# Kernel optimization log

Hardware: AMD Instinct MI355X
Metric: run time of the kernel (lower is better)

## Reference

```python
import jax, jax.numpy as jnp
import numpy as np


def _init(key, shape, fan_in):
    return jax.random.normal(key, shape, jnp.float32) * (1.0 / np.sqrt(fan_in))


def setup_inputs() -> dict:
    key = jax.random.key(0)
    ks = jax.random.split(key, 12)
    b, n, vd, ad, sd, hd = 32, 2048, 512, 128, 128, 64
    return {
        'vfeat': jax.random.normal(ks[0], (b, n, vd), jnp.float32),
        'afeat': jax.random.normal(ks[1], (b, n, ad), jnp.float32),
        'vfc_w': _init(ks[2], (ad, vd), vd), 'vfc_b': jnp.zeros((ad,), jnp.float32),
        'afc_w': _init(ks[3], (ad, ad), ad), 'afc_b': jnp.zeros((ad,), jnp.float32),
        'am_v_w': _init(ks[4], (sd, sd), sd), 'am_v_b': jnp.zeros((sd,), jnp.float32),
        'am_a_w': _init(ks[5], (sd, sd), sd), 'am_a_b': jnp.zeros((sd,), jnp.float32),
        'am_o_w': _init(ks[6], (1, sd), sd), 'am_o_b': jnp.zeros((1,), jnp.float32),
        'V_w': _init(ks[7], (hd, sd), sd), 'V_b': jnp.zeros((hd,), jnp.float32),
        'W_w': _init(ks[8], (1, hd), hd), 'W_b': jnp.zeros((1,), jnp.float32),
        'cls_w': _init(ks[9], (2, sd), sd), 'cls_b': jnp.zeros((2,), jnp.float32),
    }


def reference(vfeat, afeat, vfc_w, vfc_b, afc_w, afc_b,
              am_v_w, am_v_b, am_a_w, am_a_b, am_o_w, am_o_b,
              V_w, V_b, W_w, W_b, cls_w, cls_b):
    relu = jax.nn.relu
    # vfc / afc projections (dropout is identity in eval mode)
    vo1 = relu(jnp.einsum('bnd,kd->bnk', vfeat, vfc_w) + vfc_b)  # (b,n,128)
    ax = relu(jnp.einsum('bnd,kd->bnk', afeat, afc_w) + afc_b)   # (b,n,128)
    # AM(128): additive gated cross-modal attention: out = sigmoid(Wo tanh(Wv v + Wa a)) * a
    h = jnp.tanh(jnp.einsum('bnk,jk->bnj', vo1, am_v_w) + am_v_b
                 + jnp.einsum('bnk,jk->bnj', ax, am_a_w) + am_a_b)
    att = jax.nn.sigmoid(jnp.einsum('bnj,oj->bno', h, am_o_w) + am_o_b)  # (b,n,1)
    ffeat = att * ax + vo1  # attfeat + vo1, (b,n,128)
    # NOTE: original uses self.V for BOTH f_v and f_u (source bug kept)
    f_v = relu(jnp.einsum('bnk,hk->bnh', ffeat, V_w) + V_b)  # (b,n,64)
    f_u = f_v
    # W is affine with no nonlinearity on (fv_i + fu_j), so
    # W(fv_i + fu_j) = w.fv_i + w.fu_j + b  -- exact rank-1 decomposition
    s_v = f_v @ W_w[0]  # (b,n)
    s_u = f_u @ W_w[0]  # (b,n)
    pair = s_v[:, :, None] + s_u[:, None, :] + W_b[0]  # (b,n_i,n_j)
    p = jax.nn.softmax(pair, axis=1)  # F.softmax(scores, 0) per bag: over i
    scores = p.mean(axis=2)  # mean over j -> (b,n)
    # eval mode: training-only softmax over dim 2 skipped
    zfeat = jnp.einsum('bn,bnk->bk', scores, ffeat)  # (b,128)
    logits = zfeat @ cls_w.T + cls_b  # (b,2)
    return scores, logits
```

## Files before the change

### kernel.cpp

```cpp
#include <hip/hip_runtime.h>
#include <cstddef>
#include <cstdint>


typedef __attribute__((ext_vector_type(8))) short short8;
typedef __attribute__((ext_vector_type(4))) float float4v;

#define MFMA16(a, b, c) __builtin_amdgcn_mfma_f32_16x16x32_bf16((a), (b), (c), 0, 0, 0)

__device__ __forceinline__ unsigned short f2bf(float f) {
    union { float f; unsigned u; } v; v.f = f;
    unsigned r = (v.u + 0x7fffu + ((v.u >> 16) & 1u)) >> 16;
    return (unsigned short)r;
}
__device__ __forceinline__ float bf2f(unsigned short h) {
    union { unsigned u; float f; } v; v.u = ((unsigned)h) << 16;
    return v.f;
}
__device__ __forceinline__ float bf2f_s(short h) { return bf2f((unsigned short)h); }

__device__ __forceinline__ void bfsplit(float x, short& h, short& l) {
    union { float f; unsigned u; } v; v.f = x;
    h = (short)(v.u >> 16);
    union { unsigned u; float f; } hv; hv.u = v.u & 0xffff0000u;
    union { float f; unsigned u; } lv; lv.f = x - hv.f;
    l = (short)(lv.u >> 16);
}

__device__ __forceinline__ float tanh_fast(float x) {
    float e = __builtin_exp2f(x * 2.885390081777927f);
    return 1.f - 2.f / (e + 1.f);
}
__device__ __forceinline__ float sigmoid_fast(float x) {
    return 1.f / (1.f + __builtin_exp2f(-x * 1.4426950408889634f));
}

__device__ __forceinline__ void gload_lds16(const void* g, void* l) {
#if __has_builtin(__builtin_amdgcn_global_load_lds)
    __builtin_amdgcn_global_load_lds(
        (const __attribute__((address_space(1))) unsigned int*)g,
        (__attribute__((address_space(3))) unsigned int*)l, 16, 0, 0);
#else
    *(uint4*)l = *(const uint4*)g;
#endif
}

__global__ __launch_bounds__(256)
void prep(const float* __restrict__ vfc_w, const float* __restrict__ afc_w,
          const float* __restrict__ am_v_w, const float* __restrict__ am_a_w,
          const float* __restrict__ V_w,
          unsigned short* __restrict__ W1h, unsigned short* __restrict__ W1l,
          unsigned short* __restrict__ W1bh, unsigned short* __restrict__ W1bl,
          unsigned short* __restrict__ W2v, unsigned short* __restrict__ W2a,
          unsigned short* __restrict__ W3)
{
    int t = blockIdx.x * 256 + threadIdx.x;
    if (t < 65536) {
        int j = t & 7, lane = (t >> 3) & 63, ks = (t >> 9) & 15, nf = (t >> 13) & 7;
        int n = (lane & 15) + 16 * nf, k = ks * 32 + (lane >> 4) * 8 + j;
        float x = vfc_w[n * 512 + k];
        unsigned short h = f2bf(x);
        W1h[t] = h; W1l[t] = f2bf(x - bf2f(h));
    } else if (t < 81920) {
        int u = t - 65536;
        int j = u & 7, lane = (u >> 3) & 63, ks = (u >> 9) & 3, nf = (u >> 11) & 7;
        int n = (lane & 15) + 16 * nf, k = ks * 32 + (lane >> 4) * 8 + j;
        float x = afc_w[n * 128 + k];
        unsigned short h = f2bf(x);
        W1bh[u] = h; W1bl[u] = f2bf(x - bf2f(h));
    } else if (t < 98304) {
        int u = t - 81920;
        int j = u & 7, lane = (u >> 3) & 63, ks = (u >> 9) & 3, nf = (u >> 11) & 7;
        int n = (lane & 15) + 16 * nf, k = ks * 32 + (lane >> 4) * 8 + j;
        W2v[u] = f2bf(am_v_w[n * 128 + k]);
    } else if (t < 114688) {
        int u = t - 98304;
        int j = u & 7, lane = (u >> 3) & 63, ks = (u >> 9) & 3, nf = (u >> 11) & 7;
        int n = (lane & 15) + 16 * nf, k = ks * 32 + (lane >> 4) * 8 + j;
        W2a[u] = f2bf(am_a_w[n * 128 + k]);
    } else if (t < 122880) {
        int u = t - 114688;
        int j = u & 7, lane = (u >> 3) & 63, ks = (u >> 9) & 3, nf = (u >> 11) & 3;
        int n = (lane & 15) + 16 * nf, k = ks * 32 + (lane >> 4) * 8 + j;
        W3[u] = f2bf(V_w[n * 128 + k]);
    }
}

__global__ __launch_bounds__(256, 2)
void milA(const float* __restrict__ vfeat, const float* __restrict__ afeat,
          const float* __restrict__ vfc_b, const float* __restrict__ afc_b,
          const float* __restrict__ am_v_b, const float* __restrict__ am_a_b,
          const float* __restrict__ am_o_w, const float* __restrict__ am_o_b,
          const float* __restrict__ V_b, const float* __restrict__ W_w,
          const unsigned short* __restrict__ W1h, const unsigned short* __restrict__ W1l,
          const unsigned short* __restrict__ W1bh, const unsigned short* __restrict__ W1bl,
          const unsigned short* __restrict__ W2v, const unsigned short* __restrict__ W2a,
          const unsigned short* __restrict__ W3,
          float* __restrict__ ffeat_out, float* __restrict__ s_out)
{
    __shared__ __align__(16) unsigned short vo1s[16384];
    __shared__ __align__(16) unsigned short axs[16384];
    __shared__ __align__(16) unsigned short bstage[8192];

    const int tid = threadIdx.x;
    const int lane = tid & 63, wid = tid >> 6;
    const int lr = lane & 15, lg = lane >> 4;
    const int row0 = blockIdx.x * 128 + wid * 32;

    float b1[8], b1b[8], bias2[8], wo[8];
#pragma unroll
    for (int nf = 0; nf < 8; ++nf) {
        const int c = lr + 16 * nf;
        b1[nf] = vfc_b[c];
        b1b[nf] = afc_b[c];
        bias2[nf] = am_v_b[c] + am_a_b[c];
        wo[nf] = am_o_w[c];
    }
    const float ob = am_o_b[0];

    float4v acc1[2][8];
#pragma unroll
    for (int rf = 0; rf < 2; ++rf)
#pragma unroll
        for (int nf = 0; nf < 8; ++nf)
#pragma unroll
            for (int i = 0; i < 4; ++i) acc1[rf][nf][i] = 0.f;

    {
        const float* ap0 = vfeat + (size_t)(row0 + lr) * 512 + lg * 8;
        const float* ap1 = ap0 + (size_t)16 * 512;
        float4 acur[2][2];
        acur[0][0] = *(const float4*)(ap0);
        acur[0][1] = *(const float4*)(ap0 + 4);
        acur[1][0] = *(const float4*)(ap1);
        acur[1][1] = *(const float4*)(ap1 + 4);

        for (int ks = 0; ks < 16; ++ks) {
            __syncthreads();
#pragma unroll
            for (int i = 0; i < 4; ++i) {
                const int idx = wid * 4 + i;
                const unsigned short* src = (idx < 8)
                    ? W1h + (size_t)(idx * 16 + ks) * 512
                    : W1l + (size_t)((idx - 8) * 16 + ks) * 512;
                gload_lds16(src + (size_t)lane * 8, &bstage[idx * 512 + lane * 8]);
            }
            __syncthreads();

            float4 anxt[2][2];
            if (ks < 15) {
                anxt[0][0] = *(const float4*)(ap0 + (ks + 1) * 32);
                anxt[0][1] = *(const float4*)(ap0 + (ks + 1) * 32 + 4);
                anxt[1][0] = *(const float4*)(ap1 + (ks + 1) * 32);
                anxt[1][1] = *(const float4*)(ap1 + (ks + 1) * 32 + 4);
            }
            short8 ah[2], al[2];
#pragma unroll
            for (int rf = 0; rf < 2; ++rf) {
                const float xs[8] = {acur[rf][0].x, acur[rf][0].y, acur[rf][0].z, acur[rf][0].w,
                                     acur[rf][1].x, acur[rf][1].y, acur[rf][1].z, acur[rf][1].w};
#pragma unroll
                for (int j = 0; j < 8; ++j) {
                    short h, l; bfsplit(xs[j], h, l);
                    ah[rf][j] = h; al[rf][j] = l;
                }
            }
#pragma unroll
            for (int nf = 0; nf < 8; ++nf) {
                const short8 bh = *(const short8*)&bstage[nf * 512 + lane * 8];
                const short8 bl = *(const short8*)&bstage[4096 + nf * 512 + lane * 8];
#pragma unroll
                for (int rf = 0; rf < 2; ++rf) {
                    acc1[rf][nf] = MFMA16(ah[rf], bh, acc1[rf][nf]);
                    acc1[rf][nf] = MFMA16(ah[rf], bl, acc1[rf][nf]);
                    acc1[rf][nf] = MFMA16(al[rf], bh, acc1[rf][nf]);
                }
            }
            if (ks < 15) {
#pragma unroll
                for (int rf = 0; rf < 2; ++rf) {
                    acur[rf][0] = anxt[rf][0];
                    acur[rf][1] = anxt[rf][1];
                }
            }
        }
    }
#pragma unroll
    for (int rf = 0; rf < 2; ++rf)
#pragma unroll
        for (int nf = 0; nf < 8; ++nf)
#pragma unroll
            for (int r = 0; r < 4; ++r) {
                float v = fmaxf(acc1[rf][nf][r] + b1[nf], 0.f);
                acc1[rf][nf][r] = v;
                const int row = rf * 16 + lg * 4 + r;
                const int col = lr + 16 * nf;
                vo1s[wid * 4096 + row * 128 + (col ^ ((row & 7) << 3))] = f2bf(v);
            }

    float4v acc1b[2][8];
#pragma unroll
    for (int rf = 0; rf < 2; ++rf)
#pragma unroll
        for (int nf = 0; nf < 8; ++nf)
#pragma unroll
            for (int i = 0; i < 4; ++i) acc1b[rf][nf][i] = 0.f;

    {
        const float* ap0 = afeat + (size_t)(row0 + lr) * 128 + lg * 8;
        const float* ap1 = ap0 + (size_t)16 * 128;
        float4 acur[2][2];
        acur[0][0] = *(const float4*)(ap0);
        acur[0][1] = *(const float4*)(ap0 + 4);
        acur[1][0] = *(const float4*)(ap1);
        acur[1][1] = *(const float4*)(ap1 + 4);

        for (int ks = 0; ks < 4; ++ks) {
            __syncthreads();
#pragma unroll
            for (int i = 0; i < 4; ++i) {
                const int idx = wid * 4 + i;
                const unsigned short* src = (idx < 8)
                    ? W1bh + (size_t)(idx * 4 + ks) * 512
                    : W1bl + (size_t)((idx - 8) * 4 + ks) * 512;
                gload_lds16(src + (size_t)lane * 8, &bstage[idx * 512 + lane * 8]);
            }
            __syncthreads();

            float4 anxt[2][2];
            if (ks < 3) {
                anxt[0][0] = *(const float4*)(ap0 + (ks + 1) * 32);
                anxt[0][1] = *(const float4*)(ap0 + (ks + 1) * 32 + 4);
                anxt[1][0] = *(const float4*)(ap1 + (ks + 1) * 32);
                anxt[1][1] = *(const float4*)(ap1 + (ks + 1) * 32 + 4);
            }
            short8 ah[2], al[2];
#pragma unroll
            for (int rf = 0; rf < 2; ++rf) {
                const float xs[8] = {acur[rf][0].x, acur[rf][0].y, acur[rf][0].z, acur[rf][0].w,
                                     acur[rf][1].x, acur[rf][1].y, acur[rf][1].z, acur[rf][1].w};
#pragma unroll
                for (int j = 0; j < 8; ++j) {
                    short h, l; bfsplit(xs[j], h, l);
                    ah[rf][j] = h; al[rf][j] = l;
                }
            }
#pragma unroll
            for (int nf = 0; nf < 8; ++nf) {
                const short8 bh = *(const short8*)&bstage[nf * 512 + lane * 8];
                const short8 bl = *(const short8*)&bstage[4096 + nf * 512 + lane * 8];
#pragma unroll
                for (int rf = 0; rf < 2; ++rf) {
                    acc1b[rf][nf] = MFMA16(ah[rf], bh, acc1b[rf][nf]);
                    acc1b[rf][nf] = MFMA16(ah[rf], bl, acc1b[rf][nf]);
                    acc1b[rf][nf] = MFMA16(al[rf], bh, acc1b[rf][nf]);
                }
            }
            if (ks < 3) {
#pragma unroll
                for (int rf = 0; rf < 2; ++rf) {
                    acur[rf][0] = anxt[rf][0];
                    acur[rf][1] = anxt[rf][1];
                }
            }
        }
    }
#pragma unroll
    for (int rf = 0; rf < 2; ++rf)
#pragma unroll
        for (int nf = 0; nf < 8; ++nf)
#pragma unroll
            for (int r = 0; r < 4; ++r) {
                float v = fmaxf(acc1b[rf][nf][r] + b1b[nf], 0.f);
                acc1b[rf][nf][r] = v;
                const int row = rf * 16 + lg * 4 + r;
                const int col = lr + 16 * nf;
                axs[wid * 4096 + row * 128 + (col ^ ((row & 7) << 3))] = f2bf(v);
            }

    float4v acc2[2][8];
#pragma unroll
    for (int rf = 0; rf < 2; ++rf)
#pragma unroll
        for (int nf = 0; nf < 8; ++nf)
#pragma unroll
            for (int i = 0; i < 4; ++i) acc2[rf][nf][i] = 0.f;

    for (int ks = 0; ks < 4; ++ks) {
        __syncthreads();
#pragma unroll
        for (int i = 0; i < 2; ++i) {
            const int idx = wid * 2 + i;
            gload_lds16(W2v + (size_t)(idx * 4 + ks) * 512 + lane * 8,
                        &bstage[idx * 512 + lane * 8]);
        }
        __syncthreads();
        short8 a2[2];
#pragma unroll
        for (int rf = 0; rf < 2; ++rf) {
            const int row = rf * 16 + lr;
            a2[rf] = *(const short8*)&vo1s[wid * 4096 + row * 128 +
                                           ((ks * 32 + lg * 8) ^ ((row & 7) << 3))];
        }
#pragma unroll
        for (int nf = 0; nf < 8; ++nf) {
            const short8 b = *(const short8*)&bstage[nf * 512 + lane * 8];
#pragma unroll
            for (int rf = 0; rf < 2; ++rf) acc2[rf][nf] = MFMA16(a2[rf], b, acc2[rf][nf]);
        }
    }
    for (int ks = 0; ks < 4; ++ks) {
        __syncthreads();
#pragma unroll
        for (int i = 0; i < 2; ++i) {
            const int idx = wid * 2 + i;
            gload_lds16(W2a + (size_t)(idx * 4 + ks) * 512 + lane * 8,
                        &bstage[idx * 512 + lane * 8]);
        }
        __syncthreads();
        short8 a2[2];
#pragma unroll
        for (int rf = 0; rf < 2; ++rf) {
            const int row = rf * 16 + lr;
            a2[rf] = *(const short8*)&axs[wid * 4096 + row * 128 +
                                          ((ks * 32 + lg * 8) ^ ((row & 7) << 3))];
        }
#pragma unroll
        for (int nf = 0; nf < 8; ++nf) {
            const short8 b = *(const short8*)&bstage[nf * 512 + lane * 8];
#pragma unroll
            for (int rf = 0; rf < 2; ++rf) acc2[rf][nf] = MFMA16(a2[rf], b, acc2[rf][nf]);
        }
    }

    float attc[2][4];
#pragma unroll
    for (int rf = 0; rf < 2; ++rf)
#pragma unroll
        for (int r = 0; r < 4; ++r) {
            float p = 0.f;
#pragma unroll
            for (int nf = 0; nf < 8; ++nf)
                p += tanh_fast(acc2[rf][nf][r] + bias2[nf]) * wo[nf];
            p += __shfl_xor(p, 1);
            p += __shfl_xor(p, 2);
            p += __shfl_xor(p, 4);
            p += __shfl_xor(p, 8);
            attc[rf][r] = sigmoid_fast(p + ob);
        }

#pragma unroll
    for (int rf = 0; rf < 2; ++rf)
#pragma unroll
        for (int nf = 0; nf < 8; ++nf)
#pragma unroll
            for (int r = 0; r < 4; ++r)
                ffeat_out[(size_t)(row0 + rf * 16 + lg * 4 + r) * 128 + lr + 16 * nf] =
                    attc[rf][r] * acc1b[rf][nf][r] + acc1[rf][nf][r];

    float attv[2];
    {
        const int srcl = (lr >> 2) << 4;
#pragma unroll
        for (int rf = 0; rf < 2; ++rf) {
            const float b0 = __shfl(attc[rf][0], srcl);
            const float b1 = __shfl(attc[rf][1], srcl);
            const float b2 = __shfl(attc[rf][2], srcl);
            const float b3 = __shfl(attc[rf][3], srcl);
            attv[rf] = (lr & 2) ? ((lr & 1) ? b3 : b2) : ((lr & 1) ? b1 : b0);
        }
    }

    float4v acc3[2][4];
#pragma unroll
    for (int rf = 0; rf < 2; ++rf)
#pragma unroll
        for (int nf = 0; nf < 4; ++nf)
#pragma unroll
            for (int i = 0; i < 4; ++i) acc3[rf][nf][i] = 0.f;

    for (int ks = 0; ks < 4; ++ks) {
        __syncthreads();
        gload_lds16(W3 + (size_t)(wid * 4 + ks) * 512 + lane * 8,
                    &bstage[wid * 512 + lane * 8]);
        __syncthreads();
        short8 a3[2];
#pragma unroll
        for (int rf = 0; rf < 2; ++rf) {
            const int row = rf * 16 + lr;
            const int sidx = wid * 4096 + row * 128 + ((ks * 32 + lg * 8) ^ ((row & 7) << 3));
            const short8 x8 = *(const short8*)&axs[sidx];
            const short8 v8 = *(const short8*)&vo1s[sidx];
#pragma unroll
            for (int j = 0; j < 8; ++j) {
                float f = attv[rf] * bf2f_s(x8[j]) + bf2f_s(v8[j]);
                a3[rf][j] = (short)f2bf(f);
            }
        }
#pragma unroll
        for (int nf = 0; nf < 4; ++nf) {
            const short8 b = *(const short8*)&bstage[nf * 512 + lane * 8];
#pragma unroll
            for (int rf = 0; rf < 2; ++rf) acc3[rf][nf] = MFMA16(a3[rf], b, acc3[rf][nf]);
        }
    }

    float vb3[4], ww3[4];
#pragma unroll
    for (int nf = 0; nf < 4; ++nf) {
        const int c = lr + 16 * nf;
        vb3[nf] = V_b[c];
        ww3[nf] = W_w[c];
    }
#pragma unroll
    for (int rf = 0; rf < 2; ++rf)
#pragma unroll
        for (int r = 0; r < 4; ++r) {
            float q = 0.f;
#pragma unroll
            for (int nf = 0; nf < 4; ++nf)
                q += fmaxf(acc3[rf][nf][r] + vb3[nf], 0.f) * ww3[nf];
            q += __shfl_xor(q, 1);
            q += __shfl_xor(q, 2);
            q += __shfl_xor(q, 4);
            q += __shfl_xor(q, 8);
            if (lr == 0) s_out[row0 + rf * 16 + lg * 4 + r] = q;
        }
}

__device__ __forceinline__ float wred_sum(float v) {
#pragma unroll
    for (int m = 32; m >= 1; m >>= 1) v += __shfl_xor(v, m);
    return v;
}
__device__ __forceinline__ float wred_max(float v) {
#pragma unroll
    for (int m = 32; m >= 1; m >>= 1) v = fmaxf(v, __shfl_xor(v, m));
    return v;
}

__global__ __launch_bounds__(256)
void milB1(const float* __restrict__ s_in, float* __restrict__ scores_out)
{
    __shared__ float red[4];
    const int t = threadIdx.x, b = blockIdx.x, w = t >> 6;
    const float* sb = s_in + (size_t)b * 2048;

    float v[8];
#pragma unroll
    for (int q = 0; q < 8; ++q) v[q] = sb[q * 256 + t];
    float m = v[0];
#pragma unroll
    for (int q = 1; q < 8; ++q) m = fmaxf(m, v[q]);
    m = wred_max(m);
    if ((t & 63) == 0) red[w] = m;
    __syncthreads();
    const float bm = fmaxf(fmaxf(red[0], red[1]), fmaxf(red[2], red[3]));

    float e[8], sum = 0.f;
#pragma unroll
// ... 58 lines not shown
    const float* vfc_w  = (const float*)d_in[2];
    const float* vfc_b  = (const float*)d_in[3];
    const float* afc_w  = (const float*)d_in[4];
    const float* afc_b  = (const float*)d_in[5];
    const float* am_v_w = (const float*)d_in[6];
    const float* am_v_b = (const float*)d_in[7];
    const float* am_a_w = (const float*)d_in[8];
    const float* am_a_b = (const float*)d_in[9];
    const float* am_o_w = (const float*)d_in[10];
    const float* am_o_b = (const float*)d_in[11];
    const float* V_w    = (const float*)d_in[12];
    const float* V_b    = (const float*)d_in[13];
    const float* W_w    = (const float*)d_in[14];
    const float* cls_w  = (const float*)d_in[16];
    const float* cls_b  = (const float*)d_in[17];

    float* scores = (float*)d_out;
    float* logits = (float*)d_out + 32 * 2048;

    char* ws = (char*)d_ws;
    float* ffeat_ws = (float*)ws;
    float* s_ws     = (float*)(ws + 33554432);
    float* parts_ws = (float*)(ws + 33816576);
    unsigned short* W1h  = (unsigned short*)(ws + 33947648);
    unsigned short* W1l  = W1h + 65536;
    unsigned short* W1bh = W1l + 65536;
    unsigned short* W1bl = W1bh + 16384;
    unsigned short* W2v  = W1bl + 16384;
    unsigned short* W2a  = W2v + 16384;
    unsigned short* W3   = W2a + 16384;

    prep<<<480, 256, 0, stream>>>(vfc_w, afc_w, am_v_w, am_a_w, V_w,
                                  W1h, W1l, W1bh, W1bl, W2v, W2a, W3);
    milA<<<512, 256, 0, stream>>>(vfeat, afeat, vfc_b, afc_b, am_v_b, am_a_b,
                                  am_o_w, am_o_b, V_b, W_w,
                                  W1h, W1l, W1bh, W1bl, W2v, W2a, W3,
                                  ffeat_ws, s_ws);
    milB1<<<32, 256, 0, stream>>>(s_ws, scores);
    milB2<<<256, 256, 0, stream>>>(scores, ffeat_ws, parts_ws);
    milB3<<<32, 128, 0, stream>>>(parts_ws, cls_w, cls_b, logits);
}
```

Before: 91.96 us.

## Halve rows per wave in milA to raise occupancy and merge W2 staging loops

Each wave in milA now handles 16 rows instead of 32, so the grid doubles to 1024 blocks and LDS and register usage per block roughly halve. Launch bounds move to 3 blocks per CU. The A-operand prefetch becomes two steps deep, the W2v and W2a passes share one staged loop, and all of W3 is loaded once before the final GEMM instead of per k-step. The aim is more occupancy and fewer barriers to hide global-load latency, at the cost of reloading each weight tile for half as many rows, which doubles weight staging traffic.

```diff
diff --git a/kernel.cpp b/kernel.cpp
--- a/kernel.cpp
+++ b/kernel.cpp
@@ -86,7 +86,7 @@
     }
 }
 
-__global__ __launch_bounds__(256, 2)
+__global__ __launch_bounds__(256, 3)
 void milA(const float* __restrict__ vfeat, const float* __restrict__ afeat,
           const float* __restrict__ vfc_b, const float* __restrict__ afc_b,
           const float* __restrict__ am_v_b, const float* __restrict__ am_a_b,
@@ -98,42 +98,26 @@
           const unsigned short* __restrict__ W3,
           float* __restrict__ ffeat_out, float* __restrict__ s_out)
 {
-    __shared__ __align__(16) unsigned short vo1s[16384];
-    __shared__ __align__(16) unsigned short axs[16384];
+    __shared__ __align__(16) unsigned short vo1s[8192];
+    __shared__ __align__(16) unsigned short axs[8192];
     __shared__ __align__(16) unsigned short bstage[8192];
 
     const int tid = threadIdx.x;
     const int lane = tid & 63, wid = tid >> 6;
     const int lr = lane & 15, lg = lane >> 4;
-    const int row0 = blockIdx.x * 128 + wid * 32;
-
-    float b1[8], b1b[8], bias2[8], wo[8];
-#pragma unroll
-    for (int nf = 0; nf < 8; ++nf) {
-        const int c = lr + 16 * nf;
-        b1[nf] = vfc_b[c];
-        b1b[nf] = afc_b[c];
-        bias2[nf] = am_v_b[c] + am_a_b[c];
-        wo[nf] = am_o_w[c];
-    }
-    const float ob = am_o_b[0];
-
-    float4v acc1[2][8];
-#pragma unroll
-    for (int rf = 0; rf < 2; ++rf)
-#pragma unroll
-        for (int nf = 0; nf < 8; ++nf)
-#pragma unroll
-            for (int i = 0; i < 4; ++i) acc1[rf][nf][i] = 0.f;
+    const int row0 = blockIdx.x * 64 + wid * 16;
+
+    float4v acc1[8];
+#pragma unroll
+    for (int nf = 0; nf < 8; ++nf)
+#pragma unroll
+        for (int i = 0; i < 4; ++i) acc1[nf][i] = 0.f;
 
     {
-        const float* ap0 = vfeat + (size_t)(row0 + lr) * 512 + lg * 8;
-        const float* ap1 = ap0 + (size_t)16 * 512;
-        float4 acur[2][2];
-        acur[0][0] = *(const float4*)(ap0);
-        acur[0][1] = *(const float4*)(ap0 + 4);
-        acur[1][0] = *(const float4*)(ap1);
-        acur[1][1] = *(const float4*)(ap1 + 4);
+        const float* ap = vfeat + (size_t)(row0 + lr) * 512 + lg * 8;
+        float4 a0[2], a1[2], a2[2];
+        a0[0] = *(const float4*)(ap);      a0[1] = *(const float4*)(ap + 4);
+        a1[0] = *(const float4*)(ap + 32); a1[1] = *(const float4*)(ap + 36);
 
         for (int ks = 0; ks < 16; ++ks) {
             __syncthreads();
@@ -147,73 +131,56 @@
             }
             __syncthreads();
 
-            float4 anxt[2][2];
-            if (ks < 15) {
-                anxt[0][0] = *(const float4*)(ap0 + (ks + 1) * 32);
-                anxt[0][1] = *(const float4*)(ap0 + (ks + 1) * 32 + 4);
-                anxt[1][0] = *(const float4*)(ap1 + (ks + 1) * 32);
-                anxt[1][1] = *(const float4*)(ap1 + (ks + 1) * 32 + 4);
-            }
-            short8 ah[2], al[2];
-#pragma unroll
-            for (int rf = 0; rf < 2; ++rf) {
-                const float xs[8] = {acur[rf][0].x, acur[rf][0].y, acur[rf][0].z, acur[rf][0].w,
-                                     acur[rf][1].x, acur[rf][1].y, acur[rf][1].z, acur[rf][1].w};
+            if (ks < 14) {
+                a2[0] = *(const float4*)(ap + (ks + 2) * 32);
+                a2[1] = *(const float4*)(ap + (ks + 2) * 32 + 4);
+            }
+            short8 ah, al;
+            {
+                const float xs[8] = {a0[0].x, a0[0].y, a0[0].z, a0[0].w,
+                                     a0[1].x, a0[1].y, a0[1].z, a0[1].w};
 #pragma unroll
                 for (int j = 0; j < 8; ++j) {
                     short h, l; bfsplit(xs[j], h, l);
-                    ah[rf][j] = h; al[rf][j] = l;
+                    ah[j] = h; al[j] = l;
                 }
             }
 #pragma unroll
             for (int nf = 0; nf < 8; ++nf) {
                 const short8 bh = *(const short8*)&bstage[nf * 512 + lane * 8];
                 const short8 bl = *(const short8*)&bstage[4096 + nf * 512 + lane * 8];
-#pragma unroll
-                for (int rf = 0; rf < 2; ++rf) {
-                    acc1[rf][nf] = MFMA16(ah[rf], bh, acc1[rf][nf]);
-                    acc1[rf][nf] = MFMA16(ah[rf], bl, acc1[rf][nf]);
-                    acc1[rf][nf] = MFMA16(al[rf], bh, acc1[rf][nf]);
-                }
-            }
-            if (ks < 15) {
-#pragma unroll
-                for (int rf = 0; rf < 2; ++rf) {
-                    acur[rf][0] = anxt[rf][0];
-                    acur[rf][1] = anxt[rf][1];
-                }
-            }
-        }
-    }
-#pragma unroll
-    for (int rf = 0; rf < 2; ++rf)
-#pragma unroll
-        for (int nf = 0; nf < 8; ++nf)
-#pragma unroll
-            for (int r = 0; r < 4; ++r) {
-                float v = fmaxf(acc1[rf][nf][r] + b1[nf], 0.f);
-                acc1[rf][nf][r] = v;
-                const int row = rf * 16 + lg * 4 + r;
-                const int col = lr + 16 * nf;
-                vo1s[wid * 4096 + row * 128 + (col ^ ((row & 7) << 3))] = f2bf(v);
-            }
-
-    float4v acc1b[2][8];
-#pragma unroll
-    for (int rf = 0; rf < 2; ++rf)
-#pragma unroll
-        for (int nf = 0; nf < 8; ++nf)
-#pragma unroll
-            for (int i = 0; i < 4; ++i) acc1b[rf][nf][i] = 0.f;
+                acc1[nf] = MFMA16(ah, bh, acc1[nf]);
+                acc1[nf] = MFMA16(ah, bl, acc1[nf]);
+                acc1[nf] = MFMA16(al, bh, acc1[nf]);
+            }
+            a0[0] = a1[0]; a0[1] = a1[1];
+            a1[0] = a2[0]; a1[1] = a2[1];
+        }
+    }
+#pragma unroll
+    for (int nf = 0; nf < 8; ++nf) {
+        const float bb = vfc_b[lr + 16 * nf];
+#pragma unroll
+        for (int r = 0; r < 4; ++r) {
+            float v = fmaxf(acc1[nf][r] + bb, 0.f);
+            acc1[nf][r] = v;
+            const int row = lg * 4 + r;
+            const int col = lr + 16 * nf;
+            vo1s[wid * 2048 + row * 128 + (col ^ ((row & 7) << 3))] = f2bf(v);
+        }
+    }
+
+    float4v acc1b[8];
+#pragma unroll
+    for (int nf = 0; nf < 8; ++nf)
+#pragma unroll
+        for (int i = 0; i < 4; ++i) acc1b[nf][i] = 0.f;
 
     {
-        const float* ap0 = afeat + (size_t)(row0 + lr) * 128 + lg * 8;
-        const float* ap1 = ap0 + (size_t)16 * 128;
-        float4 acur[2][2];
-        acur[0][0] = *(const float4*)(ap0);
-        acur[0][1] = *(const float4*)(ap0 + 4);
-        acur[1][0] = *(const float4*)(ap1);
-        acur[1][1] = *(const float4*)(ap1 + 4);
+        const float* ap = afeat + (size_t)(row0 + lr) * 128 + lg * 8;
+        float4 a0[2], a1[2], a2[2];
+        a0[0] = *(const float4*)(ap);      a0[1] = *(const float4*)(ap + 4);
+        a1[0] = *(const float4*)(ap + 32); a1[1] = *(const float4*)(ap + 36);
 
         for (int ks = 0; ks < 4; ++ks) {
             __syncthreads();
@@ -227,205 +194,169 @@
             }
             __syncthreads();
 
-            float4 anxt[2][2];
-            if (ks < 3) {
-                anxt[0][0] = *(const float4*)(ap0 + (ks + 1) * 32);
-                anxt[0][1] = *(const float4*)(ap0 + (ks + 1) * 32 + 4);
-                anxt[1][0] = *(const float4*)(ap1 + (ks + 1) * 32);
-                anxt[1][1] = *(const float4*)(ap1 + (ks + 1) * 32 + 4);
-            }
-            short8 ah[2], al[2];
-#pragma unroll
-            for (int rf = 0; rf < 2; ++rf) {
-                const float xs[8] = {acur[rf][0].x, acur[rf][0].y, acur[rf][0].z, acur[rf][0].w,
-                                     acur[rf][1].x, acur[rf][1].y, acur[rf][1].z, acur[rf][1].w};
+            if (ks < 2) {
+                a2[0] = *(const float4*)(ap + (ks + 2) * 32);
+                a2[1] = *(const float4*)(ap + (ks + 2) * 32 + 4);
+            }
+            short8 ah, al;
+            {
+                const float xs[8] = {a0[0].x, a0[0].y, a0[0].z, a0[0].w,
+                                     a0[1].x, a0[1].y, a0[1].z, a0[1].w};
 #pragma unroll
                 for (int j = 0; j < 8; ++j) {
                     short h, l; bfsplit(xs[j], h, l);
-                    ah[rf][j] = h; al[rf][j] = l;
+                    ah[j] = h; al[j] = l;
                 }
             }
 #pragma unroll
             for (int nf = 0; nf < 8; ++nf) {
                 const short8 bh = *(const short8*)&bstage[nf * 512 + lane * 8];
                 const short8 bl = *(const short8*)&bstage[4096 + nf * 512 + lane * 8];
-#pragma unroll
-                for (int rf = 0; rf < 2; ++rf) {
-                    acc1b[rf][nf] = MFMA16(ah[rf], bh, acc1b[rf][nf]);
-                    acc1b[rf][nf] = MFMA16(ah[rf], bl, acc1b[rf][nf]);
-                    acc1b[rf][nf] = MFMA16(al[rf], bh, acc1b[rf][nf]);
-                }
-            }
-            if (ks < 3) {
-#pragma unroll
-                for (int rf = 0; rf < 2; ++rf) {
-                    acur[rf][0] = anxt[rf][0];
-                    acur[rf][1] = anxt[rf][1];
-                }
-            }
-        }
-    }
-#pragma unroll
-    for (int rf = 0; rf < 2; ++rf)
-#pragma unroll
-        for (int nf = 0; nf < 8; ++nf)
-#pragma unroll
-            for (int r = 0; r < 4; ++r) {
-                float v = fmaxf(acc1b[rf][nf][r] + b1b[nf], 0.f);
-                acc1b[rf][nf][r] = v;
-                const int row = rf * 16 + lg * 4 + r;
-                const int col = lr + 16 * nf;
-                axs[wid * 4096 + row * 128 + (col ^ ((row & 7) << 3))] = f2bf(v);
-            }
-
-    float4v acc2[2][8];
-#pragma unroll
-    for (int rf = 0; rf < 2; ++rf)
-#pragma unroll
-        for (int nf = 0; nf < 8; ++nf)
-#pragma unroll
-            for (int i = 0; i < 4; ++i) acc2[rf][nf][i] = 0.f;
+                acc1b[nf] = MFMA16(ah, bh, acc1b[nf]);
+                acc1b[nf] = MFMA16(ah, bl, acc1b[nf]);
+                acc1b[nf] = MFMA16(al, bh, acc1b[nf]);
+            }
+            a0[0] = a1[0]; a0[1] = a1[1];
+            a1[0] = a2[0]; a1[1] = a2[1];
+        }
+    }
+#pragma unroll
+    for (int nf = 0; nf < 8; ++nf) {
+        const float bb = afc_b[lr + 16 * nf];
+#pragma unroll
+        for (int r = 0; r < 4; ++r) {
+            float v = fmaxf(acc1b[nf][r] + bb, 0.f);
+            acc1b[nf][r] = v;
+            const int row = lg * 4 + r;
+            const int col = lr + 16 * nf;
+            axs[wid * 2048 + row * 128 + (col ^ ((row & 7) << 3))] = f2bf(v);
+        }
+    }
+
+    float4v acc2[8];
+#pragma unroll
+    for (int nf = 0; nf < 8; ++nf)
+#pragma unroll
+        for (int i = 0; i < 4; ++i) acc2[nf][i] = 0.f;
 
     for (int ks = 0; ks < 4; ++ks) {
         __syncthreads();
 #pragma unroll
-        for (int i = 0; i < 2; ++i) {
-            const int idx = wid * 2 + i;
-            gload_lds16(W2v + (size_t)(idx * 4 + ks) * 512 + lane * 8,
-                        &bstage[idx * 512 + lane * 8]);
+        for (int i = 0; i < 4; ++i) {
+            const int idx = wid * 4 + i;
+            const unsigned short* src = (idx < 8)
+                ? W2v + (size_t)(idx * 4 + ks) * 512
+                : W2a + (size_t)((idx - 8) * 4 + ks) * 512;
+            gload_lds16(src + (size_t)lane * 8, &bstage[idx * 512 + lane * 8]);
         }
         __syncthreads();
-        short8 a2[2];
-#pragma unroll
-        for (int rf = 0; rf < 2; ++rf) {
-            const int row = rf * 16 + lr;
-            a2[rf] = *(const short8*)&vo1s[wid * 4096 + row * 128 +
-                                           ((ks * 32 + lg * 8) ^ ((row & 7) << 3))];
-        }
+        const int rdoff = (ks * 32 + lg * 8) ^ ((lr & 7) << 3);
+        const short8 a2v = *(const short8*)&vo1s[wid * 2048 + lr * 128 + rdoff];
+        const short8 a2a = *(const short8*)&axs[wid * 2048 + lr * 128 + rdoff];
 #pragma unroll
         for (int nf = 0; nf < 8; ++nf) {
-            const short8 b = *(const short8*)&bstage[nf * 512 + lane * 8];
-#pragma unroll
-            for (int rf = 0; rf < 2; ++rf) acc2[rf][nf] = MFMA16(a2[rf], b, acc2[rf][nf]);
-        }
-    }
-    for (int ks = 0; ks < 4; ++ks) {
-        __syncthreads();
-#pragma unroll
-        for (int i = 0; i < 2; ++i) {
-            const int idx = wid * 2 + i;
-            gload_lds16(W2a + (size_t)(idx * 4 + ks) * 512 + lane * 8,
-                        &bstage[idx * 512 + lane * 8]);
-        }
-        __syncthreads();
-        short8 a2[2];
-#pragma unroll
-        for (int rf = 0; rf < 2; ++rf) {
-            const int row = rf * 16 + lr;
-            a2[rf] = *(const short8*)&axs[wid * 4096 + row * 128 +
-                                          ((ks * 32 + lg * 8) ^ ((row & 7) << 3))];
-        }
+            const short8 bv = *(const short8*)&bstage[nf * 512 + lane * 8];
+            const short8 ba = *(const short8*)&bstage[4096 + nf * 512 + lane * 8];
+            acc2[nf] = MFMA16(a2v, bv, acc2[nf]);
+            acc2[nf] = MFMA16(a2a, ba, acc2[nf]);
+        }
+    }
+
+    __syncthreads();
+#pragma unroll
+    for (int i = 0; i < 4; ++i) {
+        const int idx = wid * 4 + i;
+        gload_lds16(W3 + (size_t)idx * 512 + lane * 8, &bstage[idx * 512 + lane * 8]);
+    }
+
+    float attc[4];
+    {
+        float bias2[8], wo[8];
 #pragma unroll
         for (int nf = 0; nf < 8; ++nf) {
-            const short8 b = *(const short8*)&bstage[nf * 512 + lane * 8];
-#pragma unroll
-            for (int rf = 0; rf < 2; ++rf) acc2[rf][nf] = MFMA16(a2[rf], b, acc2[rf][nf]);
-        }
-    }
-
-    float attc[2][4];
-#pragma unroll
-    for (int rf = 0; rf < 2; ++rf)
+            const int c = lr + 16 * nf;
+            bias2[nf] = am_v_b[c] + am_a_b[c];
+            wo[nf] = am_o_w[c];
+        }
+        const float ob = am_o_b[0];
 #pragma unroll
         for (int r = 0; r < 4; ++r) {
             float p = 0.f;
 #pragma unroll
             for (int nf = 0; nf < 8; ++nf)
-                p += tanh_fast(acc2[rf][nf][r] + bias2[nf]) * wo[nf];
+                p += tanh_fast(acc2[nf][r] + bias2[nf]) * wo[nf];
             p += __shfl_xor(p, 1);
             p += __shfl_xor(p, 2);
             p += __shfl_xor(p, 4);
             p += __shfl_xor(p, 8);
-            attc[rf][r] = sigmoid_fast(p + ob);
-        }
-
-#pragma unroll
-    for (int rf = 0; rf < 2; ++rf)
-#pragma unroll
-        for (int nf = 0; nf < 8; ++nf)
-#pragma unroll
-            for (int r = 0; r < 4; ++r)
-                ffeat_out[(size_t)(row0 + rf * 16 + lg * 4 + r) * 128 + lr + 16 * nf] =
-                    attc[rf][r] * acc1b[rf][nf][r] + acc1[rf][nf][r];
-
-    float attv[2];
+            attc[r] = sigmoid_fast(p + ob);
+        }
+    }
+
+#pragma unroll
+    for (int nf = 0; nf < 8; ++nf)
+#pragma unroll
+        for (int r = 0; r < 4; ++r)
+            ffeat_out[(size_t)(row0 + lg * 4 + r) * 128 + lr + 16 * nf] =
+                attc[r] * acc1b[nf][r] + acc1[nf][r];
+
+    float attv;
     {
         const int srcl = (lr >> 2) << 4;
-#pragma unroll
-        for (int rf = 0; rf < 2; ++rf) {
-            const float b0 = __shfl(attc[rf][0], srcl);
-            const float b1 = __shfl(attc[rf][1], srcl);
-            const float b2 = __shfl(attc[rf][2], srcl);
-            const float b3 = __shfl(attc[rf][3], srcl);
-            attv[rf] = (lr & 2) ? ((lr & 1) ? b3 : b2) : ((lr & 1) ? b1 : b0);
-        }
-    }
-
-    float4v acc3[2][4];
-#pragma unroll
-    for (int rf = 0; rf < 2; ++rf)
-#pragma unroll
-        for (int nf = 0; nf < 4; ++nf)
-#pragma unroll
-            for (int i = 0; i < 4; ++i) acc3[rf][nf][i] = 0.f;
-
+        const float b0 = __shfl(attc[0], srcl);
+        const float b1 = __shfl(attc[1], srcl);
+        const float b2 = __shfl(attc[2], srcl);
+        const float b3 = __shfl(attc[3], srcl);
+        attv = (lr & 2) ? ((lr & 1) ? b3 : b2) : ((lr & 1) ? b1 : b0);
+    }
+
+    __syncthreads();
+
+    float4v acc3[4];
+#pragma unroll
+    for (int nf = 0; nf < 4; ++nf)
+#pragma unroll
+        for (int i = 0; i < 4; ++i) acc3[nf][i] = 0.f;
+
+#pragma unroll
     for (int ks = 0; ks < 4; ++ks) {
-        __syncthreads();
-        gload_lds16(W3 + (size_t)(wid * 4 + ks) * 512 + lane * 8,
-                    &bstage[wid * 512 + lane * 8]);
-        __syncthreads();
-        short8 a3[2];
-#pragma unroll
-        for (int rf = 0; rf < 2; ++rf) {
-            const int row = rf * 16 + lr;
-            const int sidx = wid * 4096 + row * 128 + ((ks * 32 + lg * 8) ^ ((row & 7) << 3));
-            const short8 x8 = *(const short8*)&axs[sidx];
-            const short8 v8 = *(const short8*)&vo1s[sidx];
-#pragma unroll
-            for (int j = 0; j < 8; ++j) {
-                float f = attv[rf] * bf2f_s(x8[j]) + bf2f_s(v8[j]);
-                a3[rf][j] = (short)f2bf(f);
-            }
+        const int rdoff = (ks * 32 + lg * 8) ^ ((lr & 7) << 3);
+        const short8 x8 = *(const short8*)&axs[wid * 2048 + lr * 128 + rdoff];
+        const short8 v8 = *(const short8*)&vo1s[wid * 2048 + lr * 128 + rdoff];
+        short8 a3;
+#pragma unroll
+        for (int j = 0; j < 8; ++j) {
+            float f = attv * bf2f_s(x8[j]) + bf2f_s(v8[j]);
+            a3[j] = (short)f2bf(f);
         }
 #pragma unroll
         for (int nf = 0; nf < 4; ++nf) {
-            const short8 b = *(const short8*)&bstage[nf * 512 + lane * 8];
-#pragma unroll
-            for (int rf = 0; rf < 2; ++rf) acc3[rf][nf] = MFMA16(a3[rf], b, acc3[rf][nf]);
-        }
-    }
-
-    float vb3[4], ww3[4];
-#pragma unroll
-    for (int nf = 0; nf < 4; ++nf) {
-        const int c = lr + 16 * nf;
-        vb3[nf] = V_b[c];
-        ww3[nf] = W_w[c];
-    }
-#pragma unroll
-    for (int rf = 0; rf < 2; ++rf)
+            const short8 b = *(const short8*)&bstage[(nf * 4 + ks) * 512 + lane * 8];
+            acc3[nf] = MFMA16(a3, b, acc3[nf]);
+        }
+    }
+
+    {
+        float vb3[4], ww3[4];
+#pragma unroll
+        for (int nf = 0; nf < 4; ++nf) {
+            const int c = lr + 16 * nf;
+            vb3[nf] = V_b[c];
+            ww3[nf] = W_w[c];
+        }
 #pragma unroll
         for (int r = 0; r < 4; ++r) {
             float q = 0.f;
 #pragma unroll
             for (int nf = 0; nf < 4; ++nf)
-                q += fmaxf(acc3[rf][nf][r] + vb3[nf], 0.f) * ww3[nf];
+                q += fmaxf(acc3[nf][r] + vb3[nf], 0.f) * ww3[nf];
             q += __shfl_xor(q, 1);
             q += __shfl_xor(q, 2);
             q += __shfl_xor(q, 4);
             q += __shfl_xor(q, 8);
-            if (lr == 0) s_out[row0 + rf * 16 + lg * 4 + r] = q;
-        }
+            if (lr == 0) s_out[row0 + lg * 4 + r] = q;
+        }
+    }
 }
 
 __device__ __forceinline__ float wred_sum(float v) {
@@ -550,10 +481,10 @@
 
     prep<<<480, 256, 0, stream>>>(vfc_w, afc_w, am_v_w, am_a_w, V_w,
                                   W1h, W1l, W1bh, W1bl, W2v, W2a, W3);
-    milA<<<512, 256, 0, stream>>>(vfeat, afeat, vfc_b, afc_b, am_v_b, am_a_b,
-                                  am_o_w, am_o_b, V_b, W_w,
-                                  W1h, W1l, W1bh, W1bl, W2v, W2a, W3,
-                                  ffeat_ws, s_ws);
+    milA<<<1024, 256, 0, stream>>>(vfeat, afeat, vfc_b, afc_b, am_v_b, am_a_b,
+                                   am_o_w, am_o_b, V_b, W_w,
+                                   W1h, W1l, W1bh, W1bl, W2v, W2a, W3,
+                                   ffeat_ws, s_ws);
     milB1<<<32, 256, 0, stream>>>(s_ws, scores);
     milB2<<<256, 256, 0, stream>>>(scores, ffeat_ws, parts_ws);
     milB3<<<32, 128, 0, stream>>>(parts_ws, cls_w, cls_b, logits);
```

New measurement: 88.82 us. -3.4%, faster.

## Pipeline weight staging with triple-buffered LDS and unified slice schedule in milA

Applied to the files above, without the earlier changes.

Replaces the per-k-step double-syncthreads weight staging with a triple-buffered LDS ring, a unified 25-slice schedule spanning all GEMM phases, and inline-asm activation loads kept two steps ahead, synchronized with explicit vmcnt waits and single barriers. It fuses the two AM GEMM loops into one interleaved loop and prestages W3 so the final GEMM needs no barriers. Launch bounds drop to one block per SM to afford the larger LDS and register footprint. The aim is to hide global load latency and cut barrier count, at the cost of lower occupancy and fragile hand-counted vmcnt values.

```diff
diff --git a/kernel.cpp b/kernel.cpp
--- a/kernel.cpp
+++ b/kernel.cpp
@@ -7,6 +7,9 @@
 typedef __attribute__((ext_vector_type(4))) float float4v;
 
 #define MFMA16(a, b, c) __builtin_amdgcn_mfma_f32_16x16x32_bf16((a), (b), (c), 0, 0, 0)
+#define VMCNT(n) asm volatile("s_waitcnt vmcnt(" #n ")" ::: "memory")
+#define BARRIER() __builtin_amdgcn_s_barrier()
+#define SCHED0() __builtin_amdgcn_sched_barrier(0)
 
 __device__ __forceinline__ unsigned short f2bf(float f) {
     union { float f; unsigned u; } v; v.f = f;
@@ -43,6 +46,11 @@
 #else
     *(uint4*)l = *(const uint4*)g;
 #endif
+}
+
+__device__ __forceinline__ void gload4(float4v& d, const float* p) {
+    asm volatile("global_load_dwordx4 %0, %1, off"
+                 : "=&v"(d) : "v"(p) : "memory");
 }
 
 __global__ __launch_bounds__(256)
@@ -86,7 +94,7 @@
     }
 }
 
-__global__ __launch_bounds__(256, 2)
+__global__ __launch_bounds__(256, 1)
 void milA(const float* __restrict__ vfeat, const float* __restrict__ afeat,
           const float* __restrict__ vfc_b, const float* __restrict__ afc_b,
           const float* __restrict__ am_v_b, const float* __restrict__ am_a_b,
@@ -98,25 +106,70 @@
           const unsigned short* __restrict__ W3,
           float* __restrict__ ffeat_out, float* __restrict__ s_out)
 {
+    __shared__ __align__(16) unsigned short bstage[3][8192];
     __shared__ __align__(16) unsigned short vo1s[16384];
     __shared__ __align__(16) unsigned short axs[16384];
-    __shared__ __align__(16) unsigned short bstage[8192];
 
     const int tid = threadIdx.x;
     const int lane = tid & 63, wid = tid >> 6;
     const int lr = lane & 15, lg = lane >> 4;
     const int row0 = blockIdx.x * 128 + wid * 32;
 
-    float b1[8], b1b[8], bias2[8], wo[8];
-#pragma unroll
-    for (int nf = 0; nf < 8; ++nf) {
-        const int c = lr + 16 * nf;
-        b1[nf] = vfc_b[c];
-        b1b[nf] = afc_b[c];
-        bias2[nf] = am_v_b[c] + am_a_b[c];
-        wo[nf] = am_o_w[c];
-    }
-    const float ob = am_o_b[0];
+    const float* apv0 = vfeat + (size_t)(row0 + lr) * 512 + lg * 8;
+    const float* apv1 = apv0 + (size_t)16 * 512;
+    const float* apa0 = afeat + (size_t)(row0 + lr) * 128 + lg * 8;
+    const float* apa1 = apa0 + (size_t)16 * 128;
+
+    auto stage16 = [&](const unsigned short* th, const unsigned short* tl,
+                       int nks, int ks, int buf) {
+#pragma unroll
+        for (int i = 0; i < 4; ++i) {
+            const int f = wid * 4 + i;
+            const int nf = f & 7;
+            const unsigned short* src = ((f >> 3) ? tl : th)
+                + ((size_t)(nf * nks + ks)) * 512 + (size_t)lane * 8;
+            gload_lds16(src, &bstage[buf][f * 512 + lane * 8]);
+        }
+    };
+    auto stage_slice = [&](int s, int buf) {
+        if (s < 16)      stage16(W1h,  W1l,  16, s,      buf);
+        else if (s < 20) stage16(W1bh, W1bl, 4,  s - 16, buf);
+        else if (s < 24) stage16(W2v,  W2a,  4,  s - 20, buf);
+        else if (s == 24) {
+#pragma unroll
+            for (int i = 0; i < 4; ++i) {
+                const int f = wid * 4 + i;
+                gload_lds16(W3 + (size_t)f * 512 + lane * 8,
+                            &bstage[buf][f * 512 + lane * 8]);
+            }
+        }
+    };
+
+    float4v a0[4], a1[4], a2[4];
+    auto issueA = [&](float4v (&a)[4], int b) {
+        const float *p0, *p1;
+        if (b < 16)      { p0 = apv0 + b * 32;        p1 = apv1 + b * 32; }
+        else if (b < 20) { p0 = apa0 + (b - 16) * 32; p1 = apa1 + (b - 16) * 32; }
+        else return;
+        gload4(a[0], p0); gload4(a[1], p0 + 4);
+        gload4(a[2], p1); gload4(a[3], p1 + 4);
+    };
+    auto rotA = [&]() {
+#pragma unroll
+        for (int q = 0; q < 4; ++q) { a0[q] = a1[q]; a1[q] = a2[q]; }
+    };
+    auto convA = [&](short8 (&ah)[2], short8 (&al)[2]) {
+#pragma unroll
+        for (int rf = 0; rf < 2; ++rf) {
+            const float xs[8] = {a0[rf*2][0], a0[rf*2][1], a0[rf*2][2], a0[rf*2][3],
+                                 a0[rf*2+1][0], a0[rf*2+1][1], a0[rf*2+1][2], a0[rf*2+1][3]};
+#pragma unroll
+            for (int j = 0; j < 8; ++j) {
+                short h, l; bfsplit(xs[j], h, l);
+                ah[rf][j] = h; al[rf][j] = l;
+            }
+        }
+    };
 
     float4v acc1[2][8];
 #pragma unroll
@@ -126,77 +179,50 @@
 #pragma unroll
             for (int i = 0; i < 4; ++i) acc1[rf][nf][i] = 0.f;
 
-    {
-        const float* ap0 = vfeat + (size_t)(row0 + lr) * 512 + lg * 8;
-        const float* ap1 = ap0 + (size_t)16 * 512;
-        float4 acur[2][2];
-        acur[0][0] = *(const float4*)(ap0);
-        acur[0][1] = *(const float4*)(ap0 + 4);
-        acur[1][0] = *(const float4*)(ap1);
-        acur[1][1] = *(const float4*)(ap1 + 4);
-
-        for (int ks = 0; ks < 16; ++ks) {
-            __syncthreads();
-#pragma unroll
-            for (int i = 0; i < 4; ++i) {
-                const int idx = wid * 4 + i;
-                const unsigned short* src = (idx < 8)
-                    ? W1h + (size_t)(idx * 16 + ks) * 512
-                    : W1l + (size_t)((idx - 8) * 16 + ks) * 512;
-                gload_lds16(src + (size_t)lane * 8, &bstage[idx * 512 + lane * 8]);
-            }
-            __syncthreads();
-
-            float4 anxt[2][2];
-            if (ks < 15) {
-                anxt[0][0] = *(const float4*)(ap0 + (ks + 1) * 32);
-                anxt[0][1] = *(const float4*)(ap0 + (ks + 1) * 32 + 4);
-                anxt[1][0] = *(const float4*)(ap1 + (ks + 1) * 32);
-                anxt[1][1] = *(const float4*)(ap1 + (ks + 1) * 32 + 4);
-            }
-            short8 ah[2], al[2];
+    issueA(a0, 0);
+    stage_slice(0, 0);
+    issueA(a1, 1);
+    stage_slice(1, 1);
+    VMCNT(8); SCHED0();
+    BARRIER(); SCHED0();
+
+    int rb = 0;
+    for (int ks = 0; ks < 16; ++ks) {
+        const int tb = (rb >= 1) ? rb - 1 : 2;
+        issueA(a2, ks + 2);
+        stage_slice(ks + 2, tb);
+        short8 ah[2], al[2];
+        convA(ah, al);
+#pragma unroll
+        for (int nf = 0; nf < 8; ++nf) {
+            const short8 bh = *(const short8*)&bstage[rb][nf * 512 + lane * 8];
+            const short8 bl = *(const short8*)&bstage[rb][(8 + nf) * 512 + lane * 8];
 #pragma unroll
             for (int rf = 0; rf < 2; ++rf) {
-                const float xs[8] = {acur[rf][0].x, acur[rf][0].y, acur[rf][0].z, acur[rf][0].w,
-                                     acur[rf][1].x, acur[rf][1].y, acur[rf][1].z, acur[rf][1].w};
-#pragma unroll
-                for (int j = 0; j < 8; ++j) {
-                    short h, l; bfsplit(xs[j], h, l);
-                    ah[rf][j] = h; al[rf][j] = l;
-                }
-            }
-#pragma unroll
-            for (int nf = 0; nf < 8; ++nf) {
-                const short8 bh = *(const short8*)&bstage[nf * 512 + lane * 8];
-                const short8 bl = *(const short8*)&bstage[4096 + nf * 512 + lane * 8];
-#pragma unroll
-                for (int rf = 0; rf < 2; ++rf) {
-                    acc1[rf][nf] = MFMA16(ah[rf], bh, acc1[rf][nf]);
-                    acc1[rf][nf] = MFMA16(ah[rf], bl, acc1[rf][nf]);
-                    acc1[rf][nf] = MFMA16(al[rf], bh, acc1[rf][nf]);
-                }
-            }
-            if (ks < 15) {
-#pragma unroll
-                for (int rf = 0; rf < 2; ++rf) {
-                    acur[rf][0] = anxt[rf][0];
-                    acur[rf][1] = anxt[rf][1];
-                }
-            }
-        }
-    }
-#pragma unroll
-    for (int rf = 0; rf < 2; ++rf)
-#pragma unroll
-        for (int nf = 0; nf < 8; ++nf)
+                acc1[rf][nf] = MFMA16(ah[rf], bh, acc1[rf][nf]);
+                acc1[rf][nf] = MFMA16(ah[rf], bl, acc1[rf][nf]);
+                acc1[rf][nf] = MFMA16(al[rf], bh, acc1[rf][nf]);
+            }
+        }
+        rotA();
+        VMCNT(8); SCHED0();
+        BARRIER(); SCHED0();
+        rb = (rb < 2) ? rb + 1 : 0;
+    }
+#pragma unroll
+    for (int rf = 0; rf < 2; ++rf)
+#pragma unroll
+        for (int nf = 0; nf < 8; ++nf) {
+            const float bb = vfc_b[lr + 16 * nf];
 #pragma unroll
             for (int r = 0; r < 4; ++r) {
-                float v = fmaxf(acc1[rf][nf][r] + b1[nf], 0.f);
+                float v = fmaxf(acc1[rf][nf][r] + bb, 0.f);
                 acc1[rf][nf][r] = v;
                 const int row = rf * 16 + lg * 4 + r;
                 const int col = lr + 16 * nf;
                 vo1s[wid * 4096 + row * 128 + (col ^ ((row & 7) << 3))] = f2bf(v);
             }
+        }
 
     float4v acc1b[2][8];
 #pragma unroll
@@ -206,77 +232,43 @@
 #pragma unroll
             for (int i = 0; i < 4; ++i) acc1b[rf][nf][i] = 0.f;
 
-    {
-        const float* ap0 = afeat + (size_t)(row0 + lr) * 128 + lg * 8;
-        const float* ap1 = ap0 + (size_t)16 * 128;
-        float4 acur[2][2];
-        acur[0][0] = *(const float4*)(ap0);
-        acur[0][1] = *(const float4*)(ap0 + 4);
-        acur[1][0] = *(const float4*)(ap1);
-        acur[1][1] = *(const float4*)(ap1 + 4);
-
-        for (int ks = 0; ks < 4; ++ks) {
-            __syncthreads();
-#pragma unroll
-            for (int i = 0; i < 4; ++i) {
-                const int idx = wid * 4 + i;
-                const unsigned short* src = (idx < 8)
-                    ? W1bh + (size_t)(idx * 4 + ks) * 512
-                    : W1bl + (size_t)((idx - 8) * 4 + ks) * 512;
-                gload_lds16(src + (size_t)lane * 8, &bstage[idx * 512 + lane * 8]);
-            }
-            __syncthreads();
-
-            float4 anxt[2][2];
-            if (ks < 3) {
-                anxt[0][0] = *(const float4*)(ap0 + (ks + 1) * 32);
-                anxt[0][1] = *(const float4*)(ap0 + (ks + 1) * 32 + 4);
-                anxt[1][0] = *(const float4*)(ap1 + (ks + 1) * 32);
-                anxt[1][1] = *(const float4*)(ap1 + (ks + 1) * 32 + 4);
-            }
-            short8 ah[2], al[2];
+    for (int ks = 0; ks < 4; ++ks) {
+        const int tb = (rb >= 1) ? rb - 1 : 2;
+        issueA(a2, 18 + ks);
+        stage_slice(18 + ks, tb);
+        short8 ah[2], al[2];
+        convA(ah, al);
+#pragma unroll
+        for (int nf = 0; nf < 8; ++nf) {
+            const short8 bh = *(const short8*)&bstage[rb][nf * 512 + lane * 8];
+            const short8 bl = *(const short8*)&bstage[rb][(8 + nf) * 512 + lane * 8];
 #pragma unroll
             for (int rf = 0; rf < 2; ++rf) {
-                const float xs[8] = {acur[rf][0].x, acur[rf][0].y, acur[rf][0].z, acur[rf][0].w,
-                                     acur[rf][1].x, acur[rf][1].y, acur[rf][1].z, acur[rf][1].w};
-#pragma unroll
-                for (int j = 0; j < 8; ++j) {
-                    short h, l; bfsplit(xs[j], h, l);
-                    ah[rf][j] = h; al[rf][j] = l;
-                }
-            }
-#pragma unroll
-            for (int nf = 0; nf < 8; ++nf) {
-                const short8 bh = *(const short8*)&bstage[nf * 512 + lane * 8];
-                const short8 bl = *(const short8*)&bstage[4096 + nf * 512 + lane * 8];
-#pragma unroll
-                for (int rf = 0; rf < 2; ++rf) {
-                    acc1b[rf][nf] = MFMA16(ah[rf], bh, acc1b[rf][nf]);
-                    acc1b[rf][nf] = MFMA16(ah[rf], bl, acc1b[rf][nf]);
-                    acc1b[rf][nf] = MFMA16(al[rf], bh, acc1b[rf][nf]);
-                }
-            }
-            if (ks < 3) {
-#pragma unroll
-                for (int rf = 0; rf < 2; ++rf) {
-                    acur[rf][0] = anxt[rf][0];
-                    acur[rf][1] = anxt[rf][1];
-                }
-            }
-        }
-    }
-#pragma unroll
-    for (int rf = 0; rf < 2; ++rf)
-#pragma unroll
-        for (int nf = 0; nf < 8; ++nf)
+                acc1b[rf][nf] = MFMA16(ah[rf], bh, acc1b[rf][nf]);
+                acc1b[rf][nf] = MFMA16(ah[rf], bl, acc1b[rf][nf]);
+                acc1b[rf][nf] = MFMA16(al[rf], bh, acc1b[rf][nf]);
+            }
+        }
+        rotA();
+        if (ks < 2) { VMCNT(8); } else { VMCNT(4); }
+        SCHED0();
+        BARRIER(); SCHED0();
+        rb = (rb < 2) ? rb + 1 : 0;
+    }
+#pragma unroll
+    for (int rf = 0; rf < 2; ++rf)
+#pragma unroll
+        for (int nf = 0; nf < 8; ++nf) {
+            const float bb = afc_b[lr + 16 * nf];
 #pragma unroll
             for (int r = 0; r < 4; ++r) {
-                float v = fmaxf(acc1b[rf][nf][r] + b1b[nf], 0.f);
+                float v = fmaxf(acc1b[rf][nf][r] + bb, 0.f);
                 acc1b[rf][nf][r] = v;
                 const int row = rf * 16 + lg * 4 + r;
                 const int col = lr + 16 * nf;
                 axs[wid * 4096 + row * 128 + (col ^ ((row & 7) << 3))] = f2bf(v);
             }
+        }
 
     float4v acc2[2][8];
 #pragma unroll
@@ -287,67 +279,61 @@
             for (int i = 0; i < 4; ++i) acc2[rf][nf][i] = 0.f;
 
     for (int ks = 0; ks < 4; ++ks) {
-        __syncthreads();
-#pragma unroll
-        for (int i = 0; i < 2; ++i) {
-            const int idx = wid * 2 + i;
-            gload_lds16(W2v + (size_t)(idx * 4 + ks) * 512 + lane * 8,
-                        &bstage[idx * 512 + lane * 8]);
-        }
-        __syncthreads();
-        short8 a2[2];
+        const int tb = (rb >= 1) ? rb - 1 : 2;
+        stage_slice(22 + ks, tb);
+        short8 a2v[2], a2a[2];
 #pragma unroll
         for (int rf = 0; rf < 2; ++rf) {
             const int row = rf * 16 + lr;
-            a2[rf] = *(const short8*)&vo1s[wid * 4096 + row * 128 +
-                                           ((ks * 32 + lg * 8) ^ ((row & 7) << 3))];
+            const int rdoff = (ks * 32 + lg * 8) ^ ((row & 7) << 3);
+            a2v[rf] = *(const short8*)&vo1s[wid * 4096 + row * 128 + rdoff];
+            a2a[rf] = *(const short8*)&axs[wid * 4096 + row * 128 + rdoff];
         }
 #pragma unroll
         for (int nf = 0; nf < 8; ++nf) {
-            const short8 b = *(const short8*)&bstage[nf * 512 + lane * 8];
-#pragma unroll
-            for (int rf = 0; rf < 2; ++rf) acc2[rf][nf] = MFMA16(a2[rf], b, acc2[rf][nf]);
-        }
-    }
-    for (int ks = 0; ks < 4; ++ks) {
-        __syncthreads();
-#pragma unroll
-        for (int i = 0; i < 2; ++i) {
-            const int idx = wid * 2 + i;
-            gload_lds16(W2a + (size_t)(idx * 4 + ks) * 512 + lane * 8,
-                        &bstage[idx * 512 + lane * 8]);
-        }
-        __syncthreads();
-        short8 a2[2];
-#pragma unroll
-        for (int rf = 0; rf < 2; ++rf) {
-            const int row = rf * 16 + lr;
-            a2[rf] = *(const short8*)&axs[wid * 4096 + row * 128 +
-                                          ((ks * 32 + lg * 8) ^ ((row & 7) << 3))];
-        }
+            const short8 bv = *(const short8*)&bstage[rb][nf * 512 + lane * 8];
+            const short8 ba = *(const short8*)&bstage[rb][(8 + nf) * 512 + lane * 8];
+#pragma unroll
+            for (int rf = 0; rf < 2; ++rf) {
+                acc2[rf][nf] = MFMA16(a2v[rf], bv, acc2[rf][nf]);
+                acc2[rf][nf] = MFMA16(a2a[rf], ba, acc2[rf][nf]);
+            }
+        }
+        if (ks < 3) {
+            VMCNT(4); SCHED0();
+            BARRIER(); SCHED0();
+        }
+        rb = (rb < 2) ? rb + 1 : 0;
+    }
+
+    float attc[2][4];
+    {
+        float bias2[8], wo[8];
 #pragma unroll
         for (int nf = 0; nf < 8; ++nf) {
-            const short8 b = *(const short8*)&bstage[nf * 512 + lane * 8];
-#pragma unroll
-            for (int rf = 0; rf < 2; ++rf) acc2[rf][nf] = MFMA16(a2[rf], b, acc2[rf][nf]);
-        }
-    }
-
-    float attc[2][4];
-#pragma unroll
-    for (int rf = 0; rf < 2; ++rf)
-#pragma unroll
-        for (int r = 0; r < 4; ++r) {
-            float p = 0.f;
-#pragma unroll
-            for (int nf = 0; nf < 8; ++nf)
-                p += tanh_fast(acc2[rf][nf][r] + bias2[nf]) * wo[nf];
-            p += __shfl_xor(p, 1);
-            p += __shfl_xor(p, 2);
-            p += __shfl_xor(p, 4);
-            p += __shfl_xor(p, 8);
-            attc[rf][r] = sigmoid_fast(p + ob);
-        }
+            const int c = lr + 16 * nf;
+            bias2[nf] = am_v_b[c] + am_a_b[c];
+            wo[nf] = am_o_w[c];
+        }
+        const float ob = am_o_b[0];
+#pragma unroll
+        for (int rf = 0; rf < 2; ++rf)
+#pragma unroll
+            for (int r = 0; r < 4; ++r) {
+                float p = 0.f;
+#pragma unroll
+                for (int nf = 0; nf < 8; ++nf)
+                    p += tanh_fast(acc2[rf][nf][r] + bias2[nf]) * wo[nf];
+                p += __shfl_xor(p, 1);
+                p += __shfl_xor(p, 2);
+                p += __shfl_xor(p, 4);
+                p += __shfl_xor(p, 8);
+                attc[rf][r] = sigmoid_fast(p + ob);
+            }
+    }
+
+    VMCNT(0); SCHED0();
+    BARRIER(); SCHED0();
 
 #pragma unroll
     for (int rf = 0; rf < 2; ++rf)
@@ -379,11 +365,8 @@
 #pragma unroll
             for (int i = 0; i < 4; ++i) acc3[rf][nf][i] = 0.f;
 
+#pragma unroll
     for (int ks = 0; ks < 4; ++ks) {
-        __syncthreads();
-        gload_lds16(W3 + (size_t)(wid * 4 + ks) * 512 + lane * 8,
-                    &bstage[wid * 512 + lane * 8]);
-        __syncthreads();
         short8 a3[2];
 #pragma unroll
         for (int rf = 0; rf < 2; ++rf) {
@@ -399,33 +382,35 @@
         }
 #pragma unroll
         for (int nf = 0; nf < 4; ++nf) {
-            const short8 b = *(const short8*)&bstage[nf * 512 + lane * 8];
+            const short8 b = *(const short8*)&bstage[0][(nf * 4 + ks) * 512 + lane * 8];
 #pragma unroll
             for (int rf = 0; rf < 2; ++rf) acc3[rf][nf] = MFMA16(a3[rf], b, acc3[rf][nf]);
         }
     }
 
-    float vb3[4], ww3[4];
-#pragma unroll
-    for (int nf = 0; nf < 4; ++nf) {
-        const int c = lr + 16 * nf;
-        vb3[nf] = V_b[c];
-        ww3[nf] = W_w[c];
-    }
-#pragma unroll
-    for (int rf = 0; rf < 2; ++rf)
-#pragma unroll
-        for (int r = 0; r < 4; ++r) {
-            float q = 0.f;
-#pragma unroll
-            for (int nf = 0; nf < 4; ++nf)
-                q += fmaxf(acc3[rf][nf][r] + vb3[nf], 0.f) * ww3[nf];
-            q += __shfl_xor(q, 1);
-            q += __shfl_xor(q, 2);
-            q += __shfl_xor(q, 4);
-            q += __shfl_xor(q, 8);
-            if (lr == 0) s_out[row0 + rf * 16 + lg * 4 + r] = q;
-        }
+    {
+        float vb3[4], ww3[4];
+#pragma unroll
+        for (int nf = 0; nf < 4; ++nf) {
+            const int c = lr + 16 * nf;
+            vb3[nf] = V_b[c];
+            ww3[nf] = W_w[c];
+        }
+#pragma unroll
+        for (int rf = 0; rf < 2; ++rf)
+#pragma unroll
+            for (int r = 0; r < 4; ++r) {
+                float q = 0.f;
+#pragma unroll
+                for (int nf = 0; nf < 4; ++nf)
+                    q += fmaxf(acc3[rf][nf][r] + vb3[nf], 0.f) * ww3[nf];
+                q += __shfl_xor(q, 1);
+                q += __shfl_xor(q, 2);
+                q += __shfl_xor(q, 4);
+                q += __shfl_xor(q, 8);
+                if (lr == 0) s_out[row0 + rf * 16 + lg * 4 + r] = q;
+            }
+    }
 }
 
 __device__ __forceinline__ float wred_sum(float v) {
```

New measurement: 112.6 us. 22.5% more time.
